# Kernel optimization log

Measured on AMD Instinct MI355X. Metric: run time of the kernel, lower is better.

## Reference

```python
import jax, jax.numpy as jnp
import numpy as np

N_NODES = 100000
N_LAYERS = 3


def spmm(rows, cols, vals, x):
    # sparse [N,N] @ dense [N,d] via gather + segment_sum
    msg = vals[:, None] * x[cols]  # [E, d]
    return jax.ops.segment_sum(msg, rows, num_segments=N_NODES)


def setup_inputs() -> dict:
    key = jax.random.key(0)
    k1, k2, k3, k4, k5, k6, k7 = jax.random.split(key, 7)
    E, D, B = 1600000, 64, 4096
    return {
        "embeds": jax.random.normal(k1, (N_NODES, D), dtype=jnp.float32),
        "adj_rows": jax.random.randint(k2, (E,), 0, N_NODES, dtype=jnp.int32),
        "adj_cols": jax.random.randint(k3, (E,), 0, N_NODES, dtype=jnp.int32),
        "adj_vals": jax.random.uniform(k4, (E,), dtype=jnp.float32),
        "node": jax.random.randint(k5, (B,), 0, N_NODES, dtype=jnp.int32),
        "pos_node": jax.random.randint(k6, (B,), 0, N_NODES, dtype=jnp.int32),
        "neg_node": jax.random.randint(k7, (B,), 0, N_NODES, dtype=jnp.int32),
    }


def reference(embeds, adj_rows, adj_cols, adj_vals, node, pos_node, neg_node):
    # GraphConv: multi-hop propagation with running accumulation (mean pooling fused)
    agg = embeds
    acc = embeds  # running sum of layer embeddings (hop 0)
    for _ in range(N_LAYERS):
        agg = spmm(adj_rows, adj_cols, adj_vals, agg)
        acc = acc + agg
    pooled = acc / (N_LAYERS + 1)  # aggr == 'mean'
    return (
        pooled[node],
        pooled[pos_node],
        pooled[neg_node],
        embeds[node],
        embeds[pos_node],
        embeds[neg_node],
    )
```

## Files before the change

### kernel.cpp

```cpp
#include <hip/hip_runtime.h>


#define NBUCKET 3125
#define BSHIFT  5
#define BMASK   31
#define NCHUNK  256

static __device__ __forceinline__ ushort f2bf(float f) {
    unsigned u = __float_as_uint(f);
    unsigned r = (u + 0x7fffu + ((u >> 16) & 1u)) >> 16;
    return (ushort)r;
}
static __device__ __forceinline__ float bf2f(ushort b) {
    return __uint_as_float(((unsigned)b) << 16);
}

__global__ __launch_bounds__(256) void f2bf_k(
    const float* __restrict__ in, ushort* __restrict__ out, int n4)
{
    int i = blockIdx.x * blockDim.x + threadIdx.x;
    if (i >= n4) return;
    float4 v = *(const float4*)(in + (long)i * 4);
    ushort4 o;
    o.x = f2bf(v.x); o.y = f2bf(v.y); o.z = f2bf(v.z); o.w = f2bf(v.w);
    *(ushort4*)(out + (long)i * 4) = o;
}

__global__ __launch_bounds__(1024) void count_k(
    const int* __restrict__ rows, int* __restrict__ cnt, int E, int chunkE)
{
    __shared__ unsigned h[NBUCKET];
    int c = blockIdx.x;
    for (int b = threadIdx.x; b < NBUCKET; b += 1024) h[b] = 0u;
    __syncthreads();
    int s = c * chunkE;
    int e = min(s + chunkE, E);
    for (int j = s + (int)threadIdx.x; j < e; j += 1024)
        atomicAdd(&h[rows[j] >> BSHIFT], 1u);
    __syncthreads();
    int* o = cnt + (long)c * NBUCKET;
    for (int b = threadIdx.x; b < NBUCKET; b += 1024) o[b] = (int)h[b];
}

__global__ __launch_bounds__(256) void localscan_k(
    const int* __restrict__ cnt, int* __restrict__ offs,
    int* __restrict__ totals)
{
    int b = blockIdx.x * 256 + threadIdx.x;
    if (b >= NBUCKET) return;
    int run = 0;
    #pragma unroll 8
    for (int c = 0; c < NCHUNK; ++c) {
        long i = (long)c * NBUCKET + b;
        int v = cnt[i];
        offs[i] = run;
        run += v;
    }
    totals[b] = run;
}

__global__ __launch_bounds__(1024) void scan_fused_k(
    const int* __restrict__ totals, int* __restrict__ bucket_start, int nbucket)
{
    __shared__ int sm[1024];
    __shared__ int carry_s;
    if (threadIdx.x == 0) carry_s = 0;
    __syncthreads();
    int ntile = (nbucket + 1023) / 1024;
    for (int t = 0; t < ntile; ++t) {
        int i = t * 1024 + threadIdx.x;
        int v = (i < nbucket) ? totals[i] : 0;
        sm[threadIdx.x] = v;
        __syncthreads();
        for (int off = 1; off < 1024; off <<= 1) {
            int add = (threadIdx.x >= off) ? sm[threadIdx.x - off] : 0;
            __syncthreads();
            sm[threadIdx.x] += add;
            __syncthreads();
        }
        int c0 = carry_s;
        if (i < nbucket) bucket_start[i] = c0 + sm[threadIdx.x] - v;
        __syncthreads();
        if (threadIdx.x == 1023) carry_s = c0 + sm[1023];
        __syncthreads();
    }
    if (threadIdx.x == 0) bucket_start[nbucket] = carry_s;
}

__global__ __launch_bounds__(1024) void scatter3_k(
    const int* __restrict__ rows, const int* __restrict__ cols,
    const float* __restrict__ vals, const int* __restrict__ offs,
    const int* __restrict__ bucket_start,
    int2* __restrict__ edges, int E, int chunkE)
{
    __shared__ int cur[NBUCKET];
    int c = blockIdx.x;
    const int* o = offs + (long)c * NBUCKET;
    for (int b = threadIdx.x; b < NBUCKET; b += 1024)
        cur[b] = o[b] + bucket_start[b];
    __syncthreads();
    int s = c * chunkE;
    int e = min(s + chunkE, E);
    for (int j = s + (int)threadIdx.x; j < e; j += 1024) {
        int r = rows[j];
        int pos = atomicAdd(&cur[r >> BSHIFT], 1);
        edges[pos] = make_int2(((r & BMASK) << 17) | cols[j],
                               __float_as_int(vals[j]));
    }
}

__global__ __launch_bounds__(256) void sort_bkt_k(
    const int* __restrict__ bucket_start, const int2* __restrict__ edges_in,
    int2* __restrict__ edges_out, int* __restrict__ row_start, int nbucket)
{
    __shared__ int cnt_s[32];
    __shared__ int cur_s[32];
    int bk = blockIdx.x;
    int t = (int)threadIdx.x;
    int s = bucket_start[bk];
    int e = bucket_start[bk + 1];
    if (t < 32) cnt_s[t] = 0;
    __syncthreads();
    for (int j = s + t; j < e; j += 256)
        atomicAdd(&cnt_s[(unsigned)edges_in[j].x >> 17], 1);
    __syncthreads();
    if (t == 0) {
        int run = s;
        #pragma unroll
        for (int r = 0; r < 32; ++r) {
            int c = cnt_s[r];
            cur_s[r] = run;
            row_start[bk * 32 + r] = run;
            run += c;
        }
    }
    __syncthreads();
    for (int j = s + t; j < e; j += 256) {
        int2 ed = edges_in[j];
        int pos = atomicAdd(&cur_s[(unsigned)ed.x >> 17], 1);
        edges_out[pos] = ed;
    }
    if (bk == nbucket - 1) {
        if (t == 0) row_start[nbucket * 32] = e;
        if (t < 16) edges_out[e + t] = make_int2(0, 0);
    }
}

#define GMAM(k) float p##k = ((j + k) < e ? __int_as_float(ee##k.y) : 0.f) * \
    bf2f(x[(long)(ee##k.x & 0x1FFFF) * 64 + d])

__global__ __launch_bounds__(256) void spmm_csr_k(
    const int* __restrict__ row_start, const int2* __restrict__ edges,
    const ushort* __restrict__ x, ushort* __restrict__ y, int N)
{
    int wid = __builtin_amdgcn_readfirstlane((int)(threadIdx.x >> 6));
    int r = blockIdx.x * 4 + wid;
    if (r >= N) return;
    int d = (int)(threadIdx.x & 63);
    int s = row_start[r];
    int e = row_start[r + 1];
    float a0 = 0.f, a1 = 0.f, a2 = 0.f, a3 = 0.f;
    float a4 = 0.f, a5 = 0.f, a6 = 0.f, a7 = 0.f;
    float a8 = 0.f, a9 = 0.f, a10 = 0.f, a11 = 0.f;
    float a12 = 0.f, a13 = 0.f, a14 = 0.f, a15 = 0.f;
    for (int j = s; j < e; j += 16) {
        int2 ee0  = edges[j];      int2 ee1  = edges[j + 1];
        int2 ee2  = edges[j + 2];  int2 ee3  = edges[j + 3];
        int2 ee4  = edges[j + 4];  int2 ee5  = edges[j + 5];
        int2 ee6  = edges[j + 6];  int2 ee7  = edges[j + 7];
        int2 ee8  = edges[j + 8];  int2 ee9  = edges[j + 9];
        int2 ee10 = edges[j + 10]; int2 ee11 = edges[j + 11];
        int2 ee12 = edges[j + 12]; int2 ee13 = edges[j + 13];
        int2 ee14 = edges[j + 14]; int2 ee15 = edges[j + 15];
        GMAM(0); GMAM(1); GMAM(2); GMAM(3);
        GMAM(4); GMAM(5); GMAM(6); GMAM(7);
        GMAM(8); GMAM(9); GMAM(10); GMAM(11);
        GMAM(12); GMAM(13); GMAM(14); GMAM(15);
        a0 += p0;  a1 += p1;  a2 += p2;  a3 += p3;
        a4 += p4;  a5 += p5;  a6 += p6;  a7 += p7;
        a8 += p8;  a9 += p9;  a10 += p10; a11 += p11;
        a12 += p12; a13 += p13; a14 += p14; a15 += p15;
    }
    float sum = (((a0 + a1) + (a2 + a3)) + ((a4 + a5) + (a6 + a7)))
              + (((a8 + a9) + (a10 + a11)) + ((a12 + a13) + (a14 + a15)));
    y[(long)r * 64 + d] = f2bf(sum);
}

__global__ __launch_bounds__(256) void init_out_k(
    const float* __restrict__ emb, const int* __restrict__ n0,
    const int* __restrict__ n1, const int* __restrict__ n2,
    float* __restrict__ out, int B)
{
    int tid = blockIdx.x * blockDim.x + threadIdx.x;
    int total = 3 * B * 16;
    if (tid >= total) return;
    int arr = tid / (B * 16);
    int rem = tid - arr * (B * 16);
    int b = rem >> 4;
    int d4 = rem & 15;
    const int* __restrict__ idx = (arr == 0) ? n0 : ((arr == 1) ? n1 : n2);
    float4 v = *(const float4*)(emb + (long)idx[b] * 64 + d4 * 4);
    float4 q = make_float4(0.25f * v.x, 0.25f * v.y, 0.25f * v.z, 0.25f * v.w);
    *(float4*)(out + (long)arr * B * 64 + (long)rem * 4) = q;
    *(float4*)(out + (long)(arr + 3) * B * 64 + (long)rem * 4) = v;
}

__global__ __launch_bounds__(256) void gather_add_k(
    const ushort* __restrict__ agg, const int* __restrict__ n0,
    const int* __restrict__ n1, const int* __restrict__ n2,
    float* __restrict__ out, int B)
{
    int tid = blockIdx.x * blockDim.x + threadIdx.x;
    int total = 3 * B * 16;
    if (tid >= total) return;
    int arr = tid / (B * 16);
    int rem = tid - arr * (B * 16);
    int b = rem >> 4;
    int d4 = rem & 15;
    const int* __restrict__ idx = (arr == 0) ? n0 : ((arr == 1) ? n1 : n2);
    ushort4 v = *(const ushort4*)(agg + (long)idx[b] * 64 + d4 * 4);
    float* o = out + (long)arr * B * 64 + (long)rem * 4;
    float4 cur = *(float4*)o;
    cur.x += 0.25f * bf2f(v.x); cur.y += 0.25f * bf2f(v.y);
    cur.z += 0.25f * bf2f(v.z); cur.w += 0.25f * bf2f(v.w);
    *(float4*)o = cur;
}

extern "C" void kernel_launch(void* const* d_in, const int* in_sizes, int n_in,
                              void* d_out, int out_size, void* d_ws, size_t ws_size,
                              hipStream_t stream)
{
    const float* emb  = (const float*)d_in[0];
    const int*   rows = (const int*)d_in[1];
    const int*   cols = (const int*)d_in[2];
    const float* vals = (const float*)d_in[3];
    const int*   node = (const int*)d_in[4];
    const int*   pos  = (const int*)d_in[5];
    const int*   neg  = (const int*)d_in[6];
    float* out = (float*)d_out;

    const int E = in_sizes[1];
    const int B = in_sizes[4];
    const int N = in_sizes[0] / 64;
    const size_t nd = (size_t)N * 64;
    const int chunkE = (E + NCHUNK - 1) / NCHUNK;
    const int nbucket = (N + BMASK) >> BSHIFT;

    ushort* aggA        = (ushort*)d_ws;
    ushort* aggB        = aggA + nd;
    int2*  edges        = (int2*)(aggB + nd);
    int2*  edges2       = edges + E;
    int*   cnt          = (int*)(edges2 + E + 16);
    int*   totals       = cnt + (long)NCHUNK * NBUCKET;
    int*   bucket_start = totals + NBUCKET;
    int*   row_start    = bucket_start + NBUCKET + 1;
    int*   offs         = (int*)edges2;

    const int gtotal   = 3 * B * 16;
    const int gblocks  = (gtotal + 255) / 256;
    const int cblocks  = ((int)(nd / 4) + 255) / 256;
    const int bblocks  = (nbucket + 255) / 256;
    const int rblocks  = (N + 3) / 4;

    init_out_k<<<gblocks, 256, 0, stream>>>(emb, node, pos, neg, out, B);
    f2bf_k<<<cblocks, 256, 0, stream>>>(emb, aggB, (int)(nd / 4));

    count_k<<<NCHUNK, 1024, 0, stream>>>(rows, cnt, E, chunkE);
    localscan_k<<<bblocks, 256, 0, stream>>>(cnt, offs, totals);
    scan_fused_k<<<1, 1024, 0, stream>>>(totals, bucket_start, nbucket);
    scatter3_k<<<NCHUNK, 1024, 0, stream>>>(rows, cols, vals, offs, bucket_start, edges, E, chunkE);
    sort_bkt_k<<<nbucket, 256, 0, stream>>>(bucket_start, edges, edges2, row_start, nbucket);

    spmm_csr_k<<<rblocks, 256, 0, stream>>>(row_start, edges2, aggB, aggA, N);
    gather_add_k<<<gblocks, 256, 0, stream>>>(aggA, node, pos, neg, out, B);

    spmm_csr_k<<<rblocks, 256, 0, stream>>>(row_start, edges2, aggA, aggB, N);
    gather_add_k<<<gblocks, 256, 0, stream>>>(aggB, node, pos, neg, out, B);

    spmm_csr_k<<<rblocks, 256, 0, stream>>>(row_start, edges2, aggB, aggA, N);
    gather_add_k<<<gblocks, 256, 0, stream>>>(aggA, node, pos, neg, out, B);
}
```

Measured before the change: 236.3 us.

## Process two CSR rows per wavefront with exact-length unrolled tails

The SpMM kernel now has each 64-lane wavefront handle two adjacent rows, interleaving 8-edge unrolled chunks from both rows to raise memory-level parallelism. The old 16-wide masked loop is replaced by exact tail handling (4/2/1), so padding reads and the edge-array sentinel padding are removed. This halves the number of wavefronts and adds per-row branching, which may lower occupancy or add divergence-free but serialized control overhead.

```diff
diff --git a/kernel.cpp b/kernel.cpp
--- a/kernel.cpp
+++ b/kernel.cpp
@@ -140,50 +140,101 @@
         int pos = atomicAdd(&cur_s[(unsigned)ed.x >> 17], 1);
         edges_out[pos] = ed;
     }
-    if (bk == nbucket - 1) {
-        if (t == 0) row_start[nbucket * 32] = e;
-        if (t < 16) edges_out[e + t] = make_int2(0, 0);
-    }
-}
-
-#define GMAM(k) float p##k = ((j + k) < e ? __int_as_float(ee##k.y) : 0.f) * \
-    bf2f(x[(long)(ee##k.x & 0x1FFFF) * 64 + d])
+    if (bk == nbucket - 1 && t == 0) row_start[nbucket * 32] = e;
+}
+
+#define GMA(nm, ee) float nm = __int_as_float(ee.y) * \
+    bf2f(x[(long)(ee.x & 0x1FFFF) * 64 + d])
 
 __global__ __launch_bounds__(256) void spmm_csr_k(
     const int* __restrict__ row_start, const int2* __restrict__ edges,
     const ushort* __restrict__ x, ushort* __restrict__ y, int N)
 {
     int wid = __builtin_amdgcn_readfirstlane((int)(threadIdx.x >> 6));
-    int r = blockIdx.x * 4 + wid;
-    if (r >= N) return;
+    int p = blockIdx.x * 4 + wid;
+    int rA = p * 2;
+    if (rA >= N) return;
+    int rB = rA + 1;
     int d = (int)(threadIdx.x & 63);
-    int s = row_start[r];
-    int e = row_start[r + 1];
-    float a0 = 0.f, a1 = 0.f, a2 = 0.f, a3 = 0.f;
-    float a4 = 0.f, a5 = 0.f, a6 = 0.f, a7 = 0.f;
-    float a8 = 0.f, a9 = 0.f, a10 = 0.f, a11 = 0.f;
-    float a12 = 0.f, a13 = 0.f, a14 = 0.f, a15 = 0.f;
-    for (int j = s; j < e; j += 16) {
-        int2 ee0  = edges[j];      int2 ee1  = edges[j + 1];
-        int2 ee2  = edges[j + 2];  int2 ee3  = edges[j + 3];
-        int2 ee4  = edges[j + 4];  int2 ee5  = edges[j + 5];
-        int2 ee6  = edges[j + 6];  int2 ee7  = edges[j + 7];
-        int2 ee8  = edges[j + 8];  int2 ee9  = edges[j + 9];
-        int2 ee10 = edges[j + 10]; int2 ee11 = edges[j + 11];
-        int2 ee12 = edges[j + 12]; int2 ee13 = edges[j + 13];
-        int2 ee14 = edges[j + 14]; int2 ee15 = edges[j + 15];
-        GMAM(0); GMAM(1); GMAM(2); GMAM(3);
-        GMAM(4); GMAM(5); GMAM(6); GMAM(7);
-        GMAM(8); GMAM(9); GMAM(10); GMAM(11);
-        GMAM(12); GMAM(13); GMAM(14); GMAM(15);
-        a0 += p0;  a1 += p1;  a2 += p2;  a3 += p3;
-        a4 += p4;  a5 += p5;  a6 += p6;  a7 += p7;
-        a8 += p8;  a9 += p9;  a10 += p10; a11 += p11;
-        a12 += p12; a13 += p13; a14 += p14; a15 += p15;
-    }
-    float sum = (((a0 + a1) + (a2 + a3)) + ((a4 + a5) + (a6 + a7)))
-              + (((a8 + a9) + (a10 + a11)) + ((a12 + a13) + (a14 + a15)));
-    y[(long)r * 64 + d] = f2bf(sum);
+    int sA = row_start[rA];
+    int eA = row_start[rA + 1];
+    int eB = (rB < N) ? row_start[rB + 1] : eA;
+    int sB = eA;
+    float aA0=0.f,aA1=0.f,aA2=0.f,aA3=0.f,aA4=0.f,aA5=0.f,aA6=0.f,aA7=0.f;
+    float aB0=0.f,aB1=0.f,aB2=0.f,aB3=0.f,aB4=0.f,aB5=0.f,aB6=0.f,aB7=0.f;
+    int jA = sA, jB = sB;
+    while ((jA + 8 <= eA) || (jB + 8 <= eB)) {
+        int doA = (jA + 8 <= eA);
+        int doB = (jB + 8 <= eB);
+        int2 A0,A1,A2,A3,A4,A5,A6,A7;
+        int2 B0,B1,B2,B3,B4,B5,B6,B7;
+        if (doA) {
+            A0 = edges[jA];     A1 = edges[jA + 1];
+            A2 = edges[jA + 2]; A3 = edges[jA + 3];
+            A4 = edges[jA + 4]; A5 = edges[jA + 5];
+            A6 = edges[jA + 6]; A7 = edges[jA + 7];
+        }
+        if (doB) {
+            B0 = edges[jB];     B1 = edges[jB + 1];
+            B2 = edges[jB + 2]; B3 = edges[jB + 3];
+            B4 = edges[jB + 4]; B5 = edges[jB + 5];
+            B6 = edges[jB + 6]; B7 = edges[jB + 7];
+        }
+        if (doA) {
+            GMA(pA0, A0); GMA(pA1, A1); GMA(pA2, A2); GMA(pA3, A3);
+            GMA(pA4, A4); GMA(pA5, A5); GMA(pA6, A6); GMA(pA7, A7);
+            aA0 += pA0; aA1 += pA1; aA2 += pA2; aA3 += pA3;
+            aA4 += pA4; aA5 += pA5; aA6 += pA6; aA7 += pA7;
+            jA += 8;
+        }
+        if (doB) {
+            GMA(pB0, B0); GMA(pB1, B1); GMA(pB2, B2); GMA(pB3, B3);
+            GMA(pB4, B4); GMA(pB5, B5); GMA(pB6, B6); GMA(pB7, B7);
+            aB0 += pB0; aB1 += pB1; aB2 += pB2; aB3 += pB3;
+            aB4 += pB4; aB5 += pB5; aB6 += pB6; aB7 += pB7;
+            jB += 8;
+        }
+    }
+    if (jA + 4 <= eA) {
+        int2 A0 = edges[jA], A1 = edges[jA+1], A2 = edges[jA+2], A3 = edges[jA+3];
+        GMA(pA0, A0); GMA(pA1, A1); GMA(pA2, A2); GMA(pA3, A3);
+        aA0 += pA0; aA1 += pA1; aA2 += pA2; aA3 += pA3;
+        jA += 4;
+    }
+    if (jB + 4 <= eB) {
+        int2 B0 = edges[jB], B1 = edges[jB+1], B2 = edges[jB+2], B3 = edges[jB+3];
+        GMA(pB0, B0); GMA(pB1, B1); GMA(pB2, B2); GMA(pB3, B3);
+        aB0 += pB0; aB1 += pB1; aB2 += pB2; aB3 += pB3;
+        jB += 4;
+    }
+    if (jA + 2 <= eA) {
+        int2 A0 = edges[jA], A1 = edges[jA+1];
+        GMA(pA0, A0); GMA(pA1, A1);
+        aA0 += pA0; aA1 += pA1;
+        jA += 2;
+    }
+    if (jB + 2 <= eB) {
+        int2 B0 = edges[jB], B1 = edges[jB+1];
+        GMA(pB0, B0); GMA(pB1, B1);
+        aB0 += pB0; aB1 += pB1;
+        jB += 2;
+    }
+    if (jA < eA) {
+        int2 A0 = edges[jA];
+        GMA(pA0, A0);
+        aA0 += pA0;
+    }
+    if (jB < eB) {
+        int2 B0 = edges[jB];
+        GMA(pB0, B0);
+        aB0 += pB0;
+    }
+    float sumA = ((aA0 + aA1) + (aA2 + aA3)) + ((aA4 + aA5) + (aA6 + aA7));
+    y[(long)rA * 64 + d] = f2bf(sumA);
+    if (rB < N) {
+        float sumB = ((aB0 + aB1) + (aB2 + aB3)) + ((aB4 + aB5) + (aB6 + aB7));
+        y[(long)rB * 64 + d] = f2bf(sumB);
+    }
 }
 
 __global__ __launch_bounds__(256) void init_out_k(
@@ -250,7 +301,7 @@
     ushort* aggB        = aggA + nd;
     int2*  edges        = (int2*)(aggB + nd);
     int2*  edges2       = edges + E;
-    int*   cnt          = (int*)(edges2 + E + 16);
+    int*   cnt          = (int*)(edges2 + E);
     int*   totals       = cnt + (long)NCHUNK * NBUCKET;
     int*   bucket_start = totals + NBUCKET;
     int*   row_start    = bucket_start + NBUCKET + 1;
@@ -260,7 +311,8 @@
     const int gblocks  = (gtotal + 255) / 256;
     const int cblocks  = ((int)(nd / 4) + 255) / 256;
     const int bblocks  = (nbucket + 255) / 256;
-    const int rblocks  = (N + 3) / 4;
+    const int npair    = (N + 1) / 2;
+    const int rblocks  = (npair + 3) / 4;
 
     init_out_k<<<gblocks, 256, 0, stream>>>(emb, node, pos, neg, out, B);
     f2bf_k<<<cblocks, 256, 0, stream>>>(emb, aggB, (int)(nd / 4));
```

Result: faster. 211.0 us (-10.7%).

## Split wavefront into four edge groups with 8-byte vector gathers

Applied to the files above, without the earlier changes.

The SpMM kernel now splits each 64-lane wavefront into four 16-lane groups. Each group handles a different edge and gathers a whole 128-byte bf16 row as 8-byte uint2 loads, where before each lane loaded a single 2-byte element for every edge. Partial sums are combined across groups with cross-lane shuffles, and 16 lanes write packed outputs. This cuts per-lane gather instruction count and raises bytes per load, at the cost of shuffle reductions and lane-dependent index selection.

```diff
diff --git a/kernel.cpp b/kernel.cpp
--- a/kernel.cpp
+++ b/kernel.cpp
@@ -13,6 +13,12 @@
 }
 static __device__ __forceinline__ float bf2f(ushort b) {
     return __uint_as_float(((unsigned)b) << 16);
+}
+static __device__ __forceinline__ float bflo(unsigned w) {
+    return __uint_as_float(w << 16);
+}
+static __device__ __forceinline__ float bfhi(unsigned w) {
+    return __uint_as_float(w & 0xFFFF0000u);
 }
 
 __global__ __launch_bounds__(256) void f2bf_k(
@@ -146,9 +152,6 @@
     }
 }
 
-#define GMAM(k) float p##k = ((j + k) < e ? __int_as_float(ee##k.y) : 0.f) * \
-    bf2f(x[(long)(ee##k.x & 0x1FFFF) * 64 + d])
-
 __global__ __launch_bounds__(256) void spmm_csr_k(
     const int* __restrict__ row_start, const int2* __restrict__ edges,
     const ushort* __restrict__ x, ushort* __restrict__ y, int N)
@@ -156,34 +159,63 @@
     int wid = __builtin_amdgcn_readfirstlane((int)(threadIdx.x >> 6));
     int r = blockIdx.x * 4 + wid;
     if (r >= N) return;
-    int d = (int)(threadIdx.x & 63);
+    int lane = (int)(threadIdx.x & 63);
+    int grp = lane >> 4;
+    int sub = lane & 15;
     int s = row_start[r];
     int e = row_start[r + 1];
-    float a0 = 0.f, a1 = 0.f, a2 = 0.f, a3 = 0.f;
-    float a4 = 0.f, a5 = 0.f, a6 = 0.f, a7 = 0.f;
-    float a8 = 0.f, a9 = 0.f, a10 = 0.f, a11 = 0.f;
-    float a12 = 0.f, a13 = 0.f, a14 = 0.f, a15 = 0.f;
+    const uint2* xv = (const uint2*)x;
+
+    float a00=0.f,a01=0.f,a02=0.f,a03=0.f;
+    float a10=0.f,a11=0.f,a12=0.f,a13=0.f;
+    float a20=0.f,a21=0.f,a22=0.f,a23=0.f;
+    float a30=0.f,a31=0.f,a32=0.f,a33=0.f;
+
     for (int j = s; j < e; j += 16) {
-        int2 ee0  = edges[j];      int2 ee1  = edges[j + 1];
-        int2 ee2  = edges[j + 2];  int2 ee3  = edges[j + 3];
-        int2 ee4  = edges[j + 4];  int2 ee5  = edges[j + 5];
-        int2 ee6  = edges[j + 6];  int2 ee7  = edges[j + 7];
-        int2 ee8  = edges[j + 8];  int2 ee9  = edges[j + 9];
-        int2 ee10 = edges[j + 10]; int2 ee11 = edges[j + 11];
-        int2 ee12 = edges[j + 12]; int2 ee13 = edges[j + 13];
-        int2 ee14 = edges[j + 14]; int2 ee15 = edges[j + 15];
-        GMAM(0); GMAM(1); GMAM(2); GMAM(3);
-        GMAM(4); GMAM(5); GMAM(6); GMAM(7);
-        GMAM(8); GMAM(9); GMAM(10); GMAM(11);
-        GMAM(12); GMAM(13); GMAM(14); GMAM(15);
-        a0 += p0;  a1 += p1;  a2 += p2;  a3 += p3;
-        a4 += p4;  a5 += p5;  a6 += p6;  a7 += p7;
-        a8 += p8;  a9 += p9;  a10 += p10; a11 += p11;
-        a12 += p12; a13 += p13; a14 += p14; a15 += p15;
-    }
-    float sum = (((a0 + a1) + (a2 + a3)) + ((a4 + a5) + (a6 + a7)))
-              + (((a8 + a9) + (a10 + a11)) + ((a12 + a13) + (a14 + a15)));
-    y[(long)r * 64 + d] = f2bf(sum);
+        int2 E0  = edges[j];      int2 E1  = edges[j + 1];
+        int2 E2  = edges[j + 2];  int2 E3  = edges[j + 3];
+        int2 E4  = edges[j + 4];  int2 E5  = edges[j + 5];
+        int2 E6  = edges[j + 6];  int2 E7  = edges[j + 7];
+        int2 E8  = edges[j + 8];  int2 E9  = edges[j + 9];
+        int2 E10 = edges[j + 10]; int2 E11 = edges[j + 11];
+        int2 E12 = edges[j + 12]; int2 E13 = edges[j + 13];
+        int2 E14 = edges[j + 14]; int2 E15 = edges[j + 15];
+        int c0 = E0.x & 0x1FFFF;
+        #define CS(i, Ei) \
+            int  c##i = (j + i < e) ? (Ei.x & 0x1FFFF) : c0; \
+            float v##i = (j + i < e) ? __int_as_float(Ei.y) : 0.f
+        int cc0 = c0; float v0 = (j < e) ? __int_as_float(E0.y) : 0.f; (void)cc0;
+        CS(1, E1);  CS(2, E2);  CS(3, E3);
+        CS(4, E4);  CS(5, E5);  CS(6, E6);  CS(7, E7);
+        CS(8, E8);  CS(9, E9);  CS(10, E10); CS(11, E11);
+        CS(12, E12); CS(13, E13); CS(14, E14); CS(15, E15);
+        #undef CS
+        #define G4(gi, ca, cb, cc, cd, va, vb, vc, vd, A0, A1, A2, A3) { \
+            int   cg = (grp < 2) ? ((grp & 1) ? cb : ca) : ((grp & 1) ? cd : cc); \
+            float vg = (grp < 2) ? ((grp & 1) ? vb : va) : ((grp & 1) ? vd : vc); \
+            uint2 g = xv[(long)cg * 16 + sub]; \
+            A0 += vg * bflo(g.x); A1 += vg * bfhi(g.x); \
+            A2 += vg * bflo(g.y); A3 += vg * bfhi(g.y); }
+        G4(0, c0, c1, c2, c3, v0, v1, v2, v3, a00, a01, a02, a03);
+        G4(1, c4, c5, c6, c7, v4, v5, v6, v7, a10, a11, a12, a13);
+        G4(2, c8, c9, c10, c11, v8, v9, v10, v11, a20, a21, a22, a23);
+        G4(3, c12, c13, c14, c15, v12, v13, v14, v15, a30, a31, a32, a33);
+        #undef G4
+    }
+    float k0 = (a00 + a10) + (a20 + a30);
+    float k1 = (a01 + a11) + (a21 + a31);
+    float k2 = (a02 + a12) + (a22 + a32);
+    float k3 = (a03 + a13) + (a23 + a33);
+    k0 += __shfl_xor(k0, 16, 64); k0 += __shfl_xor(k0, 32, 64);
+    k1 += __shfl_xor(k1, 16, 64); k1 += __shfl_xor(k1, 32, 64);
+    k2 += __shfl_xor(k2, 16, 64); k2 += __shfl_xor(k2, 32, 64);
+    k3 += __shfl_xor(k3, 16, 64); k3 += __shfl_xor(k3, 32, 64);
+    if (lane < 16) {
+        uint2 o;
+        o.x = (unsigned)f2bf(k0) | ((unsigned)f2bf(k1) << 16);
+        o.y = (unsigned)f2bf(k2) | ((unsigned)f2bf(k3) << 16);
+        ((uint2*)y)[(long)r * 16 + sub] = o;
+    }
 }
 
 __global__ __launch_bounds__(256) void init_out_k(
```

New measurement: 232.4 us (median of 2 runs). About the same (-1.6%).
